# Performance work log

Measured on AMD Instinct MI355X. Metric: run time of the kernel, lower is better.

## Reference

```python
import jax, jax.numpy as jnp
import numpy as np

K = 3
PAD = 1

def setup_inputs() -> dict:
    key = jax.random.key(0)
    x = jax.random.normal(key, (2, 3, 32, 128, 128), dtype=jnp.float32)
    return {"x": x}

def reference(x) -> jnp.ndarray:
    # Equivalent to F.conv3d(x, one_hot_weight, padding=PAD):
    # out[b, K^3*cin + K^2*i + K*j + l, d, h, w] = x_pad[b, cin, d+i, h+j, w+l]
    B, C, D, H, W = x.shape
    p = PAD
    xp = jnp.pad(x, ((0, 0), (0, 0), (p, p), (p, p), (p, p)))
    Do, Ho, Wo = D + 2 * p - K + 1, H + 2 * p - K + 1, W + 2 * p - K + 1
    # K^3 = 27 static slices; stacked cin-major to match the one-hot cout layout
    slices = [xp[:, :, i:i + Do, j:j + Ho, l:l + Wo]
              for i in range(K) for j in range(K) for l in range(K)]
    out = jnp.stack(slices, axis=2)            # [B, C, K^3, Do, Ho, Wo]
    return out.reshape(B, C * K ** 3, Do, Ho, Wo)
```

## Files before the change

### kernel.cpp

```cpp
#include <hip/hip_runtime.h>
#include <hip/hip_bf16.h>


#define B_  2
#define C_  3
#define D_  32
#define H_  128
#define W_  128
#define CHW ((size_t)(D_ * H_ * W_))

__global__ __launch_bounds__(256) void patch3d_kernel(const float* __restrict__ x,
                                                      float* __restrict__ out) {
    const int bc  = blockIdx.y;
    const int tid = blockIdx.x * 256 + threadIdx.x;
    const int w4  = tid & 31;
    const int h   = (tid >> 5) & 127;
    const int d   = tid >> 12;

    const float* __restrict__ src = x + (size_t)bc * CHW;
    float* __restrict__ dst = out + (size_t)bc * 27 * CHW + (size_t)tid * 4;

    float4 v[3][3];
    float  le[3][3], ri[3][3];

#pragma unroll
    for (int i = 0; i < 3; ++i) {
        const int dp = d + i - 1;
#pragma unroll
        for (int j = 0; j < 3; ++j) {
            const int hp = h + j - 1;
            float4 t = make_float4(0.f, 0.f, 0.f, 0.f);
            if (((unsigned)dp < (unsigned)D_) & ((unsigned)hp < (unsigned)H_)) {
                t = *reinterpret_cast<const float4*>(src + ((size_t)dp * H_ + hp) * W_ + w4 * 4);
            }
            float l_ = __shfl_up(t.w, 1, 64);
            float r_ = __shfl_down(t.x, 1, 64);
            if (w4 == 0)  l_ = 0.f;
            if (w4 == 31) r_ = 0.f;
            v[i][j] = t;  le[i][j] = l_;  ri[i][j] = r_;
        }
    }

#pragma unroll
    for (int i = 0; i < 3; ++i) {
#pragma unroll
        for (int j = 0; j < 3; ++j) {
            const float4 t = v[i][j];
            const float4 o0 = make_float4(le[i][j], t.x, t.y, t.z);
            const float4 o2 = make_float4(t.y, t.z, t.w, ri[i][j]);
            float* p = dst + (size_t)(i * 9 + j * 3) * CHW;
            *reinterpret_cast<float4*>(p)            = o0;
            *reinterpret_cast<float4*>(p + CHW)      = t;
            *reinterpret_cast<float4*>(p + 2 * CHW)  = o2;
        }
    }
}

extern "C" void kernel_launch(void* const* d_in, const int* in_sizes, int n_in,
                              void* d_out, int out_size, void* d_ws, size_t ws_size,
                              hipStream_t stream) {
    const float* x = (const float*)d_in[0];
    float* out = (float*)d_out;

    dim3 grid(512, B_ * C_, 1);
    dim3 block(256, 1, 1);
    patch3d_kernel<<<grid, block, 0, stream>>>(x, out);
}
```

Measured before the change: 72.76 us.

## Compute four output rows per thread to reuse loaded input rows

Each thread now produces four h rows (stride 2) instead of one. For each depth offset it loads a 9-row window in registers and reuses it across the three h offsets, which cuts redundant global loads and shuffles per output. The grid shrinks by 4x to 768 blocks, so there is less parallelism and more register pressure. Write streams keep their float4 coalescing, but each thread now issues four times as many stores.

```diff
diff --git a/kernel.cpp b/kernel.cpp
--- a/kernel.cpp
+++ b/kernel.cpp
@@ -11,47 +11,56 @@
 
 __global__ __launch_bounds__(256) void patch3d_kernel(const float* __restrict__ x,
                                                       float* __restrict__ out) {
-    const int bc  = blockIdx.y;
-    const int tid = blockIdx.x * 256 + threadIdx.x;
-    const int w4  = tid & 31;
-    const int h   = (tid >> 5) & 127;
-    const int d   = tid >> 12;
+    const int bc = blockIdx.y;
+    const int t  = blockIdx.x * 256 + threadIdx.x;
+
+    const int w4   = t & 31;
+    const int hpar = (t >> 5) & 1;
+    const int hsup = (t >> 6) & 15;
+    const int d    = t >> 10;
+
+    const int h0       = hsup * 8 + hpar;
+    const int base_row = h0 - 1;
 
     const float* __restrict__ src = x + (size_t)bc * CHW;
-    float* __restrict__ dst = out + (size_t)bc * 27 * CHW + (size_t)tid * 4;
-
-    float4 v[3][3];
-    float  le[3][3], ri[3][3];
+    float* __restrict__ dstc = out + (size_t)bc * 27 * CHW
+                                   + (size_t)d * (H_ * W_) + (size_t)h0 * W_ + w4 * 4;
 
 #pragma unroll
     for (int i = 0; i < 3; ++i) {
         const int dp = d + i - 1;
+
+        float4 R[9]; float le[9], ri[9];
+#pragma unroll
+        for (int m = 0; m < 9; ++m) {
+            const int hp = base_row + m;
+            float4 v = make_float4(0.f, 0.f, 0.f, 0.f);
+            if (((unsigned)dp < (unsigned)D_) & ((unsigned)hp < (unsigned)H_)) {
+                v = *reinterpret_cast<const float4*>(src + ((size_t)dp * H_ + hp) * W_ + w4 * 4);
+            }
+            float l_ = __shfl_up(v.w, 1, 64);
+            float r_ = __shfl_down(v.x, 1, 64);
+            if (w4 == 0)  l_ = 0.f;
+            if (w4 == 31) r_ = 0.f;
+            R[m] = v; le[m] = l_; ri[m] = r_;
+        }
+
 #pragma unroll
         for (int j = 0; j < 3; ++j) {
-            const int hp = h + j - 1;
-            float4 t = make_float4(0.f, 0.f, 0.f, 0.f);
-            if (((unsigned)dp < (unsigned)D_) & ((unsigned)hp < (unsigned)H_)) {
-                t = *reinterpret_cast<const float4*>(src + ((size_t)dp * H_ + hp) * W_ + w4 * 4);
+#pragma unroll
+            for (int l = 0; l < 3; ++l) {
+                float* p = dstc + (size_t)(i * 9 + j * 3 + l) * CHW;
+#pragma unroll
+                for (int k = 0; k < 4; ++k) {
+                    const int m = 2 * k + j;
+                    const float4 v = R[m];
+                    float4 o;
+                    if (l == 0)      o = make_float4(le[m], v.x, v.y, v.z);
+                    else if (l == 1) o = v;
+                    else             o = make_float4(v.y, v.z, v.w, ri[m]);
+                    *reinterpret_cast<float4*>(p + k * 256) = o;
+                }
             }
-            float l_ = __shfl_up(t.w, 1, 64);
-            float r_ = __shfl_down(t.x, 1, 64);
-            if (w4 == 0)  l_ = 0.f;
-            if (w4 == 31) r_ = 0.f;
-            v[i][j] = t;  le[i][j] = l_;  ri[i][j] = r_;
-        }
-    }
-
-#pragma unroll
-    for (int i = 0; i < 3; ++i) {
-#pragma unroll
-        for (int j = 0; j < 3; ++j) {
-            const float4 t = v[i][j];
-            const float4 o0 = make_float4(le[i][j], t.x, t.y, t.z);
-            const float4 o2 = make_float4(t.y, t.z, t.w, ri[i][j]);
-            float* p = dst + (size_t)(i * 9 + j * 3) * CHW;
-            *reinterpret_cast<float4*>(p)            = o0;
-            *reinterpret_cast<float4*>(p + CHW)      = t;
-            *reinterpret_cast<float4*>(p + 2 * CHW)  = o2;
         }
     }
 }
@@ -62,7 +71,7 @@
     const float* x = (const float*)d_in[0];
     float* out = (float*)d_out;
 
-    dim3 grid(512, B_ * C_, 1);
+    dim3 grid(128, B_ * C_, 1);
     dim3 block(256, 1, 1);
     patch3d_kernel<<<grid, block, 0, stream>>>(x, out);
 }
```

Result: faster. 67.10 us (median of 2 runs) (-7.8%).
